# Performance work log

Measured on AMD Instinct MI355X. Metric: run time of the kernel, lower is better.

Reference implementation:

```python
import jax, jax.numpy as jnp
import numpy as np

N = 100000      # nodes
E = 1600000     # edges (avg degree 16)
IN_DIM = 128
HID = 128
OUT = 10
EPS = 1e-5      # BatchNorm eps


def _lin(key, fan_in, fan_out):
    return jax.random.normal(key, (fan_in, fan_out), jnp.float32) * (1.0 / np.sqrt(fan_in))


def setup_inputs() -> dict:
    key = jax.random.key(0)
    ks = jax.random.split(key, 8)
    x = jax.random.normal(ks[0], (N, IN_DIM), jnp.float32)
    edge_index = jax.random.randint(ks[1], (2, E), 0, N, dtype=jnp.int64)
    return {
        "x": x,
        "edge_index": edge_index,
        "W0": _lin(ks[2], IN_DIM, HID), "b0": jnp.zeros((HID,), jnp.float32),
        "g0": jnp.ones((HID,), jnp.float32), "be0": jnp.zeros((HID,), jnp.float32),
        "W1": _lin(ks[3], HID, HID), "b1": jnp.zeros((HID,), jnp.float32),
        "g1": jnp.ones((HID,), jnp.float32), "be1": jnp.zeros((HID,), jnp.float32),
        "W2": _lin(ks[4], HID, OUT), "b2": jnp.zeros((OUT,), jnp.float32),
    }


def gcn_conv(x, W, b, src, dst, n):
    # PyG GCNConv: add self-loops, symmetric normalization D^-1/2 A D^-1/2.
    # deg includes the self-loop (+1).
    e = src.shape[0]
    deg = jax.ops.segment_sum(jnp.ones((e,), x.dtype), dst, num_segments=n) + 1.0
    dinv = jax.lax.rsqrt(deg)                     # deg >= 1 always
    norm = dinv[src] * dinv[dst]                  # [E]
    h = x @ W                                     # [N, out]
    msgs = h[src] * norm[:, None]                 # gather + scale, [E, out]
    agg = jax.ops.segment_sum(msgs, dst, num_segments=n)
    agg = agg + h * (dinv * dinv)[:, None]        # self-loop contribution
    return agg + b


def batch_norm(x, gamma, beta):
    mu = jnp.mean(x, axis=0)
    var = jnp.mean(jnp.square(x - mu), axis=0)    # biased var, as torch BN training
    return gamma * (x - mu) * jax.lax.rsqrt(var + EPS) + beta


def reference(x, edge_index, W0, b0, g0, be0, W1, b1, g1, be1, W2, b2):
    src, dst = edge_index[0], edge_index[1]
    h = jax.nn.relu(batch_norm(gcn_conv(x, W0, b0, src, dst, N), g0, be0))
    h = jax.nn.relu(batch_norm(gcn_conv(h, W1, b1, src, dst, N), g1, be1))
    return gcn_conv(h, W2, b2, src, dst, N)
```

## Files before the change

kernel.cpp:

```cpp
#include <hip/hip_runtime.h>
#include <hip/hip_bf16.h>

static constexpr int NN  = 100000;
static constexpr int NE  = 1600000;
static constexpr int DIM = 128;
static constexpr int OC  = 10;
static constexpr int BK  = 64;
static constexpr float BN_EPS = 1e-5f;
static constexpr float INVN   = 1.0f / (float)NN;

typedef unsigned short ushortT;
typedef unsigned int uintT;
typedef __attribute__((ext_vector_type(8))) short short8;
typedef __attribute__((ext_vector_type(4))) float floatx4;

__device__ __forceinline__ ushortT f2bf(float f) {
    union { float f; unsigned int i; } c;
    c.f = f;
    unsigned int r = c.i + 0x7FFFu + ((c.i >> 16) & 1u);
    return (ushortT)(r >> 16);
}

__device__ __forceinline__ uintT pack2(float lo, float hi) {
    return (uintT)f2bf(lo) | ((uintT)f2bf(hi) << 16);
}

__device__ __forceinline__ float4 f4fma(const float4 w, const float s, const float4 acc) {
    float4 r;
    r.x = fmaf(w.x, s, acc.x);
    r.y = fmaf(w.y, s, acc.y);
    r.z = fmaf(w.z, s, acc.z);
    r.w = fmaf(w.w, s, acc.w);
    return r;
}

__device__ __forceinline__ void acc8(const uint4 u, float* a) {
    a[0] += __uint_as_float(u.x << 16);
    a[1] += __uint_as_float(u.x & 0xFFFF0000u);
    a[2] += __uint_as_float(u.y << 16);
    a[3] += __uint_as_float(u.y & 0xFFFF0000u);
    a[4] += __uint_as_float(u.z << 16);
    a[5] += __uint_as_float(u.z & 0xFFFF0000u);
    a[6] += __uint_as_float(u.w << 16);
    a[7] += __uint_as_float(u.w & 0xFFFF0000u);
}

__device__ __forceinline__ void fma8(const uint4 u, float s, float* a) {
    a[0] = fmaf(__uint_as_float(u.x << 16),          s, a[0]);
    a[1] = fmaf(__uint_as_float(u.x & 0xFFFF0000u),  s, a[1]);
    a[2] = fmaf(__uint_as_float(u.y << 16),          s, a[2]);
    a[3] = fmaf(__uint_as_float(u.y & 0xFFFF0000u),  s, a[3]);
    a[4] = fmaf(__uint_as_float(u.z << 16),          s, a[4]);
    a[5] = fmaf(__uint_as_float(u.z & 0xFFFF0000u),  s, a[5]);
    a[6] = fmaf(__uint_as_float(u.w << 16),          s, a[6]);
    a[7] = fmaf(__uint_as_float(u.w & 0xFFFF0000u),  s, a[7]);
}

__device__ __forceinline__ void unp8(const uint4 u, float* a) {
    a[0] = __uint_as_float(u.x << 16);
    a[1] = __uint_as_float(u.x & 0xFFFF0000u);
    a[2] = __uint_as_float(u.y << 16);
    a[3] = __uint_as_float(u.y & 0xFFFF0000u);
    a[4] = __uint_as_float(u.z << 16);
    a[5] = __uint_as_float(u.z & 0xFFFF0000u);
    a[6] = __uint_as_float(u.w << 16);
    a[7] = __uint_as_float(u.w & 0xFFFF0000u);
}

__global__ void k_wt(const float* __restrict__ W0, const float* __restrict__ W1,
                     ushortT* __restrict__ WT0, ushortT* __restrict__ WT1,
                     float* __restrict__ stats) {
    int i = blockIdx.x * 256 + threadIdx.x;
    if (i < 512) stats[i] = 0.f;
    int half = i >> 14, r = i & 16383;
    int n = r >> 7, k = r & 127;
    if (half == 0) WT0[r] = f2bf(W0[k * 128 + n]);
    else           WT1[r] = f2bf(W1[k * 128 + n]);
}

__global__ __launch_bounds__(256, 8)
void k_fused(const int* __restrict__ src, const int* __restrict__ dst,
             int* __restrict__ cnt, int* __restrict__ bucket,
             const float* __restrict__ x, const ushortT* __restrict__ WT,
             ushortT* __restrict__ outb)
{
    const int idx = blockIdx.x;
    const int m = idx / 3, r3 = idx - 3 * m;
    if (r3 < 2) {
        int e = (2 * m + r3) * 256 + threadIdx.x;
        if (e < NE) {
            int t = dst[e];
            int slot = atomicAdd(&cnt[t], 1);
            if (slot < BK)
                __hip_atomic_store(&bucket[(size_t)t * BK + slot], src[e],
                                   __ATOMIC_RELAXED, __HIP_MEMORY_SCOPE_AGENT);
        }
        return;
    }
    __shared__ ushortT XS[32 * 136];
    const int tid  = threadIdx.x;
    const int row0 = m * 32;

    #pragma unroll
    for (int i = 0; i < 4; ++i) {
        int id2 = tid + 256 * i;
        int rr = id2 >> 5, c4 = id2 & 31;
        int grow = row0 + rr;
        float4 v = {0.f, 0.f, 0.f, 0.f};
        if (grow < NN) v = ((const float4*)(x + (size_t)grow * DIM))[c4];
        ushort4 o;
        o.x = f2bf(v.x); o.y = f2bf(v.y); o.z = f2bf(v.z); o.w = f2bf(v.w);
        *(ushort4*)(XS + rr * 136 + c4 * 4) = o;
    }
    __syncthreads();

    const int w    = tid >> 6;
    const int lane = tid & 63;
    const int q    = lane >> 4;
    const int mr   = lane & 15;
    const int rw   = (w >> 1) * 16;
    const int ch   = (w & 1) * 64;

    floatx4 acc[4];
    #pragma unroll
    for (int t = 0; t < 4; ++t) { acc[t][0] = 0.f; acc[t][1] = 0.f; acc[t][2] = 0.f; acc[t][3] = 0.f; }

    #pragma unroll
    for (int c = 0; c < 4; ++c) {
        short8 a = *(const short8*)(XS + (rw + mr) * 136 + c * 32 + q * 8);
        #pragma unroll
        for (int t = 0; t < 4; ++t) {
            short8 b = *(const short8*)(WT + (size_t)(ch + t * 16 + mr) * 128 + c * 32 + q * 8);
            acc[t] = __builtin_amdgcn_mfma_f32_16x16x32_bf16(a, b, acc[t], 0, 0, 0);
        }
    }

    #pragma unroll
    for (int rr = 0; rr < 4; ++rr) {
        int grow = row0 + rw + q * 4 + rr;
        if (grow < NN) {
            #pragma unroll
            for (int t = 0; t < 4; ++t)
                outb[(size_t)grow * DIM + ch + t * 16 + mr] = f2bf(acc[t][rr]);
        }
    }
}

__global__ void k_dinv(const int* __restrict__ cnt, float* __restrict__ dinv, int n) {
    int i = blockIdx.x * 256 + threadIdx.x;
    if (i < n) dinv[i] = rsqrtf((float)cnt[i] + 1.0f);
}

template <bool EDGE_SCALE>
__global__ __launch_bounds__(256)
void k_agg_wide(const ushortT* __restrict__ hb, const int* __restrict__ cnt,
                const int* __restrict__ bucket, const float* __restrict__ dinv,
                const float* __restrict__ bias, ushortT* __restrict__ outBb,
                float* __restrict__ stats)
{
    const int lane = threadIdx.x & 63;
    const int w    = threadIdx.x >> 6;
    const int sg   = lane >> 4;
    const int f    = lane & 15;
    const int wid  = blockIdx.x * 4 + w;
    const int nW   = gridDim.x * 4;
    const uint4* h4 = (const uint4*)hb;

    float bl[8];
    #pragma unroll
    for (int i = 0; i < 8; ++i) bl[i] = bias[f * 8 + i];

    float ssum[8], ssq[8];
    #pragma unroll
    for (int i = 0; i < 8; ++i) { ssum[i] = 0.f; ssq[i] = 0.f; }

    for (int n = wid; n < NN; n += nW) {
        int d = cnt[n];
        if (d > BK) d = BK;
        const int* bp = bucket + (size_t)n * BK;
        float a[8];
        #pragma unroll
        for (int i = 0; i < 8; ++i) a[i] = 0.f;

        int j = 0;
        for (; j + 8 <= d; j += 8) {
            int s0 = bp[j + sg];
            int s1 = bp[j + 4 + sg];
            uint4 u0 = h4[(size_t)s0 * 16 + f];
            uint4 u1 = h4[(size_t)s1 * 16 + f];
            if (EDGE_SCALE) {
                float d0 = dinv[s0], d1 = dinv[s1];
                fma8(u0, d0, a);
                fma8(u1, d1, a);
            } else {
                acc8(u0, a);
                acc8(u1, a);
            }
        }
        for (; j < d; j += 4) {
            int e = j + sg;
            if (e < d) {
                int s0 = bp[e];
                uint4 u = h4[(size_t)s0 * 16 + f];
                if (EDGE_SCALE) fma8(u, dinv[s0], a);
                else            acc8(u, a);
            }
        }
        #pragma unroll
        for (int i = 0; i < 8; ++i) {
            a[i] += __shfl_xor(a[i], 16);
            a[i] += __shfl_xor(a[i], 32);
        }
        if (lane < 16) {
            uint4 us = h4[(size_t)n * 16 + f];
            float di = dinv[n];
            if (EDGE_SCALE) fma8(us, di, a);
            else            acc8(us, a);
            float v[8];
            #pragma unroll
            for (int i = 0; i < 8; ++i) v[i] = fmaf(di, a[i], bl[i]);
            uint4 o;
            o.x = pack2(v[0], v[1]);
            o.y = pack2(v[2], v[3]);
            o.z = pack2(v[4], v[5]);
            o.w = pack2(v[6], v[7]);
            ((uint4*)(outBb + (size_t)n * DIM))[f] = o;
            #pragma unroll
            for (int i = 0; i < 8; ++i) {
                ssum[i] += v[i];
                ssq[i]  = fmaf(v[i], v[i], ssq[i]);
            }
        }
    }

    __shared__ float ls[4 * 128], lq[4 * 128];
    if (lane < 16) {
        #pragma unroll
        for (int i = 0; i < 8; ++i) {
            ls[w * 128 + f * 8 + i] = ssum[i];
            lq[w * 128 + f * 8 + i] = ssq[i];
        }
    }
    __syncthreads();
    int t = threadIdx.x;
    if (t < 128) {
        float a = ls[t] + ls[128 + t] + ls[256 + t] + ls[384 + t];
        float b = lq[t] + lq[128 + t] + lq[256 + t] + lq[384 + t];
        unsafeAtomicAdd(&stats[t], a);
        unsafeAtomicAdd(&stats[128 + t], b);
    }
}

__global__ __launch_bounds__(256)
void k_mm128_l1(const ushortT* __restrict__ inb, const ushortT* __restrict__ WT,
                const float* __restrict__ stats, const float* __restrict__ g,
                const float* __restrict__ be, const float* __restrict__ dinv,
                ushortT* __restrict__ outb)
{
    __shared__ ushortT XS[64 * 136];
    __shared__ float CA[128], CD[128];
    const int tid  = threadIdx.x;
    const int row0 = blockIdx.x * 64;

    if (tid < 128) {
        float mu  = stats[tid] * INVN;
        float var = stats[128 + tid] * INVN - mu * mu;
        float a = g[tid] * rsqrtf(var + BN_EPS);
        CA[tid] = a;
        CD[tid] = be[tid] - mu * a;
    }
    __syncthreads();

    #pragma unroll
    for (int i = 0; i < 4; ++i) {
        int idx = tid + 256 * i;
        int r = idx >> 4, c8 = idx & 15;
        int grow = row0 + r;
        uint4 u = {0, 0, 0, 0};
        if (grow < NN) u = ((const uint4*)(inb + (size_t)grow * DIM))[c8];
        float v[8];
        unp8(u, v);
        #pragma unroll
        for (int k = 0; k < 8; ++k)
            v[k] = fmaxf(0.f, fmaf(v[k], CA[c8 * 8 + k], CD[c8 * 8 + k]));
        uint4 o;
        o.x = pack2(v[0], v[1]);
        o.y = pack2(v[2], v[3]);
        o.z = pack2(v[4], v[5]);
        o.w = pack2(v[6], v[7]);
        *(uint4*)(XS + r * 136 + c8 * 8) = o;
    }
    __syncthreads();

    const int w    = tid >> 6;
    const int lane = tid & 63;
    const int q    = lane >> 4;
    const int mr   = lane & 15;
    const int rw   = w * 16;

    floatx4 acc[8];
    #pragma unroll
    for (int t = 0; t < 8; ++t) { acc[t][0] = 0.f; acc[t][1] = 0.f; acc[t][2] = 0.f; acc[t][3] = 0.f; }

    #pragma unroll
    for (int c = 0; c < 4; ++c) {
        short8 a = *(const short8*)(XS + (rw + mr) * 136 + c * 32 + q * 8);
        #pragma unroll
        for (int t = 0; t < 8; ++t) {
            short8 b = *(const short8*)(WT + (size_t)(t * 16 + mr) * 128 + c * 32 + q * 8);
            acc[t] = __builtin_amdgcn_mfma_f32_16x16x32_bf16(a, b, acc[t], 0, 0, 0);
        }
    }

    #pragma unroll
    for (int r = 0; r < 4; ++r) {
        int grow = row0 + rw + q * 4 + r;
        if (grow < NN) {
            float di = dinv[grow];
            #pragma unroll
            for (int t = 0; t < 8; ++t) {
                outb[(size_t)grow * DIM + t * 16 + mr] = f2bf(acc[t][r] * di);
            }
        }
    }
}

__global__ __launch_bounds__(128)
void k_mm_l2(const ushortT* __restrict__ inb, const float* __restrict__ W2,
             const float* __restrict__ stats, const float* __restrict__ g,
             const float* __restrict__ be, const float* __restrict__ dinv,
             ushortT* __restrict__ Cb)
{
    __shared__ float WL[128 * 16];
    __shared__ float XS[32 * 128];
    __shared__ float CA[128], CD[128];
    const int tid  = threadIdx.x;
    const int row0 = blockIdx.x * 32;

    {
        float mu  = stats[tid] * INVN;
        float var = stats[128 + tid] * INVN - mu * mu;
        float a = g[tid] * rsqrtf(var + BN_EPS);
        CA[tid] = a;
        CD[tid] = be[tid] - mu * a;
    }
    for (int idx = tid; idx < 128 * 16; idx += 128) {
        int k = idx >> 4, c = idx & 15;
        WL[idx] = (c < OC) ? W2[k * OC + c] : 0.0f;
    }
    __syncthreads();

    #pragma unroll
    for (int i = 0; i < 4; ++i) {
        int idx = tid + 128 * i;
        int r = idx >> 4, c8 = idx & 15;
        uint4 u = ((const uint4*)(inb + (size_t)(row0 + r) * DIM))[c8];
        float v[8];
        unp8(u, v);
        float* xp = XS + r * 128 + c8 * 8;
        #pragma unroll
        for (int k = 0; k < 8; ++k)
            xp[k] = fmaxf(0.f, fmaf(v[k], CA[c8 * 8 + k], CD[c8 * 8 + k]));
    }
    __syncthreads();

    const int cg = tid & 3;
    const int rg = tid >> 2;
    float4 acc = {0, 0, 0, 0};
    const float4* XS4 = (const float4*)XS;
    const float4* WL4 = (const float4*)WL;
    for (int k = 0; k < 128; k += 4) {
        float4 w0 = WL4[(k + 0) * 4 + cg];
        float4 w1 = WL4[(k + 1) * 4 + cg];
        float4 w2 = WL4[(k + 2) * 4 + cg];
        float4 w3 = WL4[(k + 3) * 4 + cg];
        float4 x = XS4[rg * 32 + (k >> 2)];
        acc = f4fma(w0, x.x, f4fma(w1, x.y, f4fma(w2, x.z, f4fma(w3, x.w, acc))));
    }
    float di = dinv[row0 + rg];
    uint2 o;
    o.x = pack2(acc.x * di, acc.y * di);
    o.y = pack2(acc.z * di, acc.w * di);
    ((uint2*)(Cb + ((size_t)row0 + rg) * 16))[cg] = o;
}

__global__ __launch_bounds__(256)
void k_agg10(const ushortT* __restrict__ Cb, const int* __restrict__ cnt,
             const int* __restrict__ bucket, const float* __restrict__ dinv,
             const float* __restrict__ b2, float* __restrict__ out)
{
    const int lane = threadIdx.x & 63;
    const int sg   = lane >> 3;
    const int f    = lane & 7;
    const int wid  = (blockIdx.x * 256 + threadIdx.x) >> 6;
    const int nW   = gridDim.x * 4;
    const uintT* Cu = (const uintT*)Cb;

    for (int n = wid; n < NN; n += nW) {
        int d = cnt[n];
        if (d > BK) d = BK;
        const int* bp = bucket + (size_t)n * BK;
        float a0 = 0.f, a1 = 0.f;
        for (int j = sg; j < d; j += 8) {
            uintT u = Cu[(size_t)bp[j] * 8 + f];
            a0 += __uint_as_float(u << 16);
            a1 += __uint_as_float(u & 0xFFFF0000u);
        }
        a0 += __shfl_xor(a0, 8);  a1 += __shfl_xor(a1, 8);
        a0 += __shfl_xor(a0, 16); a1 += __shfl_xor(a1, 16);
        a0 += __shfl_xor(a0, 32); a1 += __shfl_xor(a1, 32);
        if (lane < 8) {
            uintT us = Cu[(size_t)n * 8 + f];
            a0 += __uint_as_float(us << 16);
            a1 += __uint_as_float(us & 0xFFFF0000u);
            float di = dinv[n];
            if (2 * f < OC) {
                float2 o;
                o.x = fmaf(di, a0, b2[2 * f]);
                o.y = fmaf(di, a1, b2[2 * f + 1]);
                *(float2*)(out + (size_t)n * OC + 2 * f) = o;
            }
        }
    }
}

extern "C" void kernel_launch(void* const* d_in, const int* in_sizes, int n_in,
                              void* d_out, int out_size, void* d_ws, size_t ws_size,
                              hipStream_t stream) {
    const float* x    = (const float*)d_in[0];
    const int*   ei   = (const int*)d_in[1];
    const int*   srcv = ei;
    const int*   dstv = ei + NE;
    const float* W0  = (const float*)d_in[2];
    const float* b0  = (const float*)d_in[3];
    const float* g0  = (const float*)d_in[4];
    const float* be0 = (const float*)d_in[5];
    const float* W1  = (const float*)d_in[6];
    const float* b1  = (const float*)d_in[7];
    const float* g1  = (const float*)d_in[8];
    const float* be1 = (const float*)d_in[9];
    const float* W2  = (const float*)d_in[10];
    const float* b2  = (const float*)d_in[11];
    float* out = (float*)d_out;

    float* base   = (float*)d_ws;
    int*   cnt    = (int*)base;
    float* dinv   = base + NN;
    float* stats  = base + 2 * NN;
    ushortT* WT0  = (ushortT*)(base + 2 * NN + 512);
    ushortT* WT1  = (ushortT*)(base + 2 * NN + 8704);
    int*   bucket = (int*)(base + 2 * NN + 16896);
    ushortT* A_bf = (ushortT*)(base + 2 * NN + 16896 + (size_t)NN * BK);
    ushortT* B_bf = A_bf + (size_t)NN * DIM;
    ushortT* Cb   = A_bf;

    hipMemsetAsync(cnt, 0, NN * sizeof(int), stream);

    k_wt<<<128, 256, 0, stream>>>(W0, W1, WT0, WT1, stats);

    k_fused<<<9375, 256, 0, stream>>>(srcv, dstv, cnt, bucket, x, WT0, A_bf);
    k_dinv<<<(NN + 255) / 256, 256, 0, stream>>>(cnt, dinv, NN);

    k_agg_wide<true><<<2048, 256, 0, stream>>>(A_bf, cnt, bucket, dinv, b0, B_bf, stats);

    k_mm128_l1<<<(NN + 63) / 64, 256, 0, stream>>>(B_bf, WT1, stats, g0, be0, dinv, A_bf);
    k_agg_wide<false><<<2048, 256, 0, stream>>>(A_bf, cnt, bucket, dinv, b1, B_bf, stats + 256);

    k_mm_l2<<<NN / 32, 128, 0, stream>>>(B_bf, W2, stats + 256, g1, be1, dinv, Cb);
    k_agg10<<<1024, 256, 0, stream>>>(Cb, cnt, bucket, dinv, b2, out);
}
```

Before: 560.5 us.

## Store hidden features in feature-sliced layout and aggregate per slice for cache locality

The GEMM outputs now write features in 8 slices of 16 columns each ([slice][node][16]), and the aggregation kernel assigns each block one slice and a contiguous node range, with 4 lanes per node. Each slice's working set (about 3.2 MB) is intended to fit in L2, so the random neighbour gathers hit cache more often than gathers over full 256-byte rows. In exchange, gathers shrink to 8 bytes per lane, the bucket indices are re-read once per slice, and the node-per-16-lane scheduling can diverge on degree imbalance.

```diff
diff --git a/kernel.cpp b/kernel.cpp
--- a/kernel.cpp
+++ b/kernel.cpp
@@ -9,6 +9,9 @@
 static constexpr float BN_EPS = 1e-5f;
 static constexpr float INVN   = 1.0f / (float)NN;
 
+static constexpr int NPB = (NN + 255) / 256;
+static constexpr int NPW = (NPB + 3) / 4;
+
 typedef unsigned short ushortT;
 typedef unsigned int uintT;
 typedef __attribute__((ext_vector_type(8))) short short8;
@@ -34,26 +37,11 @@
     return r;
 }
 
-__device__ __forceinline__ void acc8(const uint4 u, float* a) {
-    a[0] += __uint_as_float(u.x << 16);
-    a[1] += __uint_as_float(u.x & 0xFFFF0000u);
-    a[2] += __uint_as_float(u.y << 16);
-    a[3] += __uint_as_float(u.y & 0xFFFF0000u);
-    a[4] += __uint_as_float(u.z << 16);
-    a[5] += __uint_as_float(u.z & 0xFFFF0000u);
-    a[6] += __uint_as_float(u.w << 16);
-    a[7] += __uint_as_float(u.w & 0xFFFF0000u);
-}
-
-__device__ __forceinline__ void fma8(const uint4 u, float s, float* a) {
+__device__ __forceinline__ void fma4(const uint2 u, float s, float* a) {
     a[0] = fmaf(__uint_as_float(u.x << 16),          s, a[0]);
     a[1] = fmaf(__uint_as_float(u.x & 0xFFFF0000u),  s, a[1]);
     a[2] = fmaf(__uint_as_float(u.y << 16),          s, a[2]);
     a[3] = fmaf(__uint_as_float(u.y & 0xFFFF0000u),  s, a[3]);
-    a[4] = fmaf(__uint_as_float(u.z << 16),          s, a[4]);
-    a[5] = fmaf(__uint_as_float(u.z & 0xFFFF0000u),  s, a[5]);
-    a[6] = fmaf(__uint_as_float(u.w << 16),          s, a[6]);
-    a[7] = fmaf(__uint_as_float(u.w & 0xFFFF0000u),  s, a[7]);
 }
 
 __device__ __forceinline__ void unp8(const uint4 u, float* a) {
@@ -140,8 +128,9 @@
         int grow = row0 + rw + q * 4 + rr;
         if (grow < NN) {
             #pragma unroll
-            for (int t = 0; t < 4; ++t)
-                outb[(size_t)grow * DIM + ch + t * 16 + mr] = f2bf(acc[t][rr]);
+            for (int t = 0; t < 4; ++t) {
+                outb[(size_t)((ch >> 4) + t) * (NN * 16) + (size_t)grow * 16 + mr] = f2bf(acc[t][rr]);
+            }
         }
     }
 }
@@ -151,103 +140,89 @@
     if (i < n) dinv[i] = rsqrtf((float)cnt[i] + 1.0f);
 }
 
-template <bool EDGE_SCALE>
+template <bool ES>
 __global__ __launch_bounds__(256)
-void k_agg_wide(const ushortT* __restrict__ hb, const int* __restrict__ cnt,
-                const int* __restrict__ bucket, const float* __restrict__ dinv,
-                const float* __restrict__ bias, ushortT* __restrict__ outBb,
-                float* __restrict__ stats)
+void k_agg_slice(const ushortT* __restrict__ hb, const int* __restrict__ cnt,
+                 const int* __restrict__ bucket, const float* __restrict__ dinv,
+                 const float* __restrict__ bias, ushortT* __restrict__ outB,
+                 float* __restrict__ stats)
 {
+    const int s    = blockIdx.x & 7;
+    const int b    = blockIdx.x >> 3;
     const int lane = threadIdx.x & 63;
     const int w    = threadIdx.x >> 6;
-    const int sg   = lane >> 4;
-    const int f    = lane & 15;
-    const int wid  = blockIdx.x * 4 + w;
-    const int nW   = gridDim.x * 4;
-    const uint4* h4 = (const uint4*)hb;
-
-    float bl[8];
-    #pragma unroll
-    for (int i = 0; i < 8; ++i) bl[i] = bias[f * 8 + i];
-
-    float ssum[8], ssq[8];
-    #pragma unroll
-    for (int i = 0; i < 8; ++i) { ssum[i] = 0.f; ssq[i] = 0.f; }
-
-    for (int n = wid; n < NN; n += nW) {
-        int d = cnt[n];
-        if (d > BK) d = BK;
-        const int* bp = bucket + (size_t)n * BK;
-        float a[8];
-        #pragma unroll
-        for (int i = 0; i < 8; ++i) a[i] = 0.f;
-
-        int j = 0;
-        for (; j + 8 <= d; j += 8) {
-            int s0 = bp[j + sg];
-            int s1 = bp[j + 4 + sg];
-            uint4 u0 = h4[(size_t)s0 * 16 + f];
-            uint4 u1 = h4[(size_t)s1 * 16 + f];
-            if (EDGE_SCALE) {
-                float d0 = dinv[s0], d1 = dinv[s1];
-                fma8(u0, d0, a);
-                fma8(u1, d1, a);
-            } else {
-                acc8(u0, a);
-                acc8(u1, a);
+    const int ql   = lane >> 2;
+    const int fl   = lane & 3;
+    const ushortT* hsl = hb + (size_t)s * (NN * 16);
+
+    const int bStart = b * NPB;
+    const int bEnd   = (bStart + NPB < NN) ? bStart + NPB : NN;
+    const int wStart = bStart + w * NPW;
+    const int wEnd   = (wStart + NPW < bEnd) ? wStart + NPW : bEnd;
+
+    float bl[4];
+    #pragma unroll
+    for (int i = 0; i < 4; ++i) bl[i] = bias[s * 16 + fl * 4 + i];
+
+    float ssum[4] = {0.f, 0.f, 0.f, 0.f}, ssq[4] = {0.f, 0.f, 0.f, 0.f};
+
+    for (int nb = wStart; nb < wEnd; nb += 16) {
+        const int  n  = nb + ql;
+        const bool nv = (n < wEnd);
+        int d = 0;
+        if (nv) { d = cnt[n]; if (d > BK) d = BK; }
+        const int* bp = bucket + (size_t)(nv ? n : 0) * BK;
+
+        float a[4] = {0.f, 0.f, 0.f, 0.f};
+        for (int j = 0; ; j += 2) {
+            if (!__any(j < d)) break;
+            if (j < d) {
+                int2 pv = *(const int2*)(bp + j);
+                bool e1 = (j + 1 < d);
+                int s0 = pv.x;
+                int s1 = e1 ? pv.y : n;
+                uint2 u0 = *(const uint2*)(hsl + ((size_t)s0 << 4) + (fl << 2));
+                uint2 u1 = *(const uint2*)(hsl + ((size_t)s1 << 4) + (fl << 2));
+                float w0, w1;
+                if (ES) { w0 = dinv[s0]; w1 = e1 ? dinv[s1] : 0.f; }
+                else    { w0 = 1.f;      w1 = e1 ? 1.f      : 0.f; }
+                fma4(u0, w0, a);
+                fma4(u1, w1, a);
             }
         }
-        for (; j < d; j += 4) {
-            int e = j + sg;
-            if (e < d) {
-                int s0 = bp[e];
-                uint4 u = h4[(size_t)s0 * 16 + f];
-                if (EDGE_SCALE) fma8(u, dinv[s0], a);
-                else            acc8(u, a);
-            }
-        }
-        #pragma unroll
-        for (int i = 0; i < 8; ++i) {
-            a[i] += __shfl_xor(a[i], 16);
-            a[i] += __shfl_xor(a[i], 32);
-        }
-        if (lane < 16) {
-            uint4 us = h4[(size_t)n * 16 + f];
+        if (nv) {
+            uint2 us = *(const uint2*)(hsl + ((size_t)n << 4) + (fl << 2));
             float di = dinv[n];
-            if (EDGE_SCALE) fma8(us, di, a);
-            else            acc8(us, a);
-            float v[8];
+            fma4(us, ES ? di : 1.f, a);
+            float v[4];
             #pragma unroll
-            for (int i = 0; i < 8; ++i) v[i] = fmaf(di, a[i], bl[i]);
-            uint4 o;
+            for (int i = 0; i < 4; ++i) v[i] = fmaf(di, a[i], bl[i]);
+            uint2 o;
             o.x = pack2(v[0], v[1]);
             o.y = pack2(v[2], v[3]);
-            o.z = pack2(v[4], v[5]);
-            o.w = pack2(v[6], v[7]);
-            ((uint4*)(outBb + (size_t)n * DIM))[f] = o;
+            *(uint2*)(outB + (size_t)n * DIM + s * 16 + (fl << 2)) = o;
             #pragma unroll
-            for (int i = 0; i < 8; ++i) {
+            for (int i = 0; i < 4; ++i) {
                 ssum[i] += v[i];
                 ssq[i]  = fmaf(v[i], v[i], ssq[i]);
             }
         }
     }
 
-    __shared__ float ls[4 * 128], lq[4 * 128];
-    if (lane < 16) {
-        #pragma unroll
-        for (int i = 0; i < 8; ++i) {
-            ls[w * 128 + f * 8 + i] = ssum[i];
-            lq[w * 128 + f * 8 + i] = ssq[i];
-        }
-    }
-    __syncthreads();
-    int t = threadIdx.x;
-    if (t < 128) {
-        float a = ls[t] + ls[128 + t] + ls[256 + t] + ls[384 + t];
-        float b = lq[t] + lq[128 + t] + lq[256 + t] + lq[384 + t];
-        unsafeAtomicAdd(&stats[t], a);
-        unsafeAtomicAdd(&stats[128 + t], b);
+    #pragma unroll
+    for (int m = 4; m <= 32; m <<= 1) {
+        #pragma unroll
+        for (int i = 0; i < 4; ++i) {
+            ssum[i] += __shfl_xor(ssum[i], m);
+            ssq[i]  += __shfl_xor(ssq[i], m);
+        }
+    }
+    if (lane < 4) {
+        #pragma unroll
+        for (int i = 0; i < 4; ++i) {
+            unsafeAtomicAdd(&stats[s * 16 + fl * 4 + i], ssum[i]);
+            unsafeAtomicAdd(&stats[128 + s * 16 + fl * 4 + i], ssq[i]);
+        }
     }
 }
 
@@ -319,7 +294,7 @@
             float di = dinv[grow];
             #pragma unroll
             for (int t = 0; t < 8; ++t) {
-                outb[(size_t)grow * DIM + t * 16 + mr] = f2bf(acc[t][r] * di);
+                outb[(size_t)t * (NN * 16) + (size_t)grow * 16 + mr] = f2bf(acc[t][r] * di);
             }
         }
     }
@@ -461,10 +436,10 @@
     k_fused<<<9375, 256, 0, stream>>>(srcv, dstv, cnt, bucket, x, WT0, A_bf);
     k_dinv<<<(NN + 255) / 256, 256, 0, stream>>>(cnt, dinv, NN);
 
-    k_agg_wide<true><<<2048, 256, 0, stream>>>(A_bf, cnt, bucket, dinv, b0, B_bf, stats);
+    k_agg_slice<true><<<2048, 256, 0, stream>>>(A_bf, cnt, bucket, dinv, b0, B_bf, stats);
 
     k_mm128_l1<<<(NN + 63) / 64, 256, 0, stream>>>(B_bf, WT1, stats, g0, be0, dinv, A_bf);
-    k_agg_wide<false><<<2048, 256, 0, stream>>>(A_bf, cnt, bucket, dinv, b1, B_bf, stats + 256);
+    k_agg_slice<false><<<2048, 256, 0, stream>>>(A_bf, cnt, bucket, dinv, b1, B_bf, stats + 256);
 
     k_mm_l2<<<NN / 32, 128, 0, stream>>>(B_bf, W2, stats + 256, g1, be1, dinv, Cb);
     k_agg10<<<1024, 256, 0, stream>>>(Cb, cnt, bucket, dinv, b2, out);
```

Measured after the change: 771.5 us. 37.7% more time.

## Pad neighbor buckets to a sentinel row and aggregate two nodes per wave

Applied to the files above, without the earlier changes.

Edge bucketing now processes four edges per thread using vectorised int4 loads of src/dst. Each bucket is padded to a multiple of 16 with a sentinel index pointing at an added zero row, which has zero dinv. This lets aggregation read indices as int4 with no tail branches. Each wave now handles two nodes at once with eight independent gathers in flight, raising memory-level parallelism, at the cost of extra padded gathers and more registers.

```diff
diff --git a/kernel.cpp b/kernel.cpp
--- a/kernel.cpp
+++ b/kernel.cpp
@@ -69,9 +69,10 @@
 
 __global__ void k_wt(const float* __restrict__ W0, const float* __restrict__ W1,
                      ushortT* __restrict__ WT0, ushortT* __restrict__ WT1,
-                     float* __restrict__ stats) {
+                     float* __restrict__ stats, ushortT* __restrict__ hz) {
     int i = blockIdx.x * 256 + threadIdx.x;
     if (i < 512) stats[i] = 0.f;
+    if (i < DIM) hz[(size_t)NN * DIM + i] = 0;
     int half = i >> 14, r = i & 16383;
     int n = r >> 7, k = r & 127;
     if (half == 0) WT0[r] = f2bf(W0[k * 128 + n]);
@@ -85,18 +86,32 @@
              ushortT* __restrict__ outb)
 {
     const int idx = blockIdx.x;
-    const int m = idx / 3, r3 = idx - 3 * m;
-    if (r3 < 2) {
-        int e = (2 * m + r3) * 256 + threadIdx.x;
-        if (e < NE) {
-            int t = dst[e];
-            int slot = atomicAdd(&cnt[t], 1);
-            if (slot < BK)
-                __hip_atomic_store(&bucket[(size_t)t * BK + slot], src[e],
+    const int qq = idx / 3;
+    if (idx - 3 * qq == 0) {
+        int e0 = qq * 1024 + threadIdx.x * 4;
+        if (e0 < NE) {
+            int4 dv = *(const int4*)(dst + e0);
+            int4 sv = *(const int4*)(src + e0);
+            int t0 = atomicAdd(&cnt[dv.x], 1);
+            int t1 = atomicAdd(&cnt[dv.y], 1);
+            int t2 = atomicAdd(&cnt[dv.z], 1);
+            int t3 = atomicAdd(&cnt[dv.w], 1);
+            if (t0 < BK)
+                __hip_atomic_store(&bucket[(size_t)dv.x * BK + t0], sv.x,
                                    __ATOMIC_RELAXED, __HIP_MEMORY_SCOPE_AGENT);
+            if (t1 < BK)
+                __hip_atomic_store(&bucket[(size_t)dv.y * BK + t1], sv.y,
+                                   __ATOMIC_RELAXED, __HIP_MEMORY_SCOPE_AGENT);
+            if (t2 < BK)
+                __hip_atomic_store(&bucket[(size_t)dv.z * BK + t2], sv.z,
+                                   __ATOMIC_RELAXED, __HIP_MEMORY_SCOPE_AGENT);
+            if (t3 < BK)
+                __hip_atomic_store(&bucket[(size_t)dv.w * BK + t3], sv.w,
+                                   __ATOMIC_RELAXED, __HIP_MEMORY_SCOPE_AGENT);
         }
         return;
     }
+    const int m = idx - qq - 1;
     __shared__ ushortT XS[32 * 136];
     const int tid  = threadIdx.x;
     const int row0 = m * 32;
@@ -146,9 +161,19 @@
     }
 }
 
-__global__ void k_dinv(const int* __restrict__ cnt, float* __restrict__ dinv, int n) {
+__global__ void k_dinv(const int* __restrict__ cnt, float* __restrict__ dinv,
+                       int* __restrict__ bucket) {
     int i = blockIdx.x * 256 + threadIdx.x;
-    if (i < n) dinv[i] = rsqrtf((float)cnt[i] + 1.0f);
+    if (i < NN) {
+        int d = cnt[i];
+        dinv[i] = rsqrtf((float)d + 1.0f);
+        int dc = d > BK ? BK : d;
+        int dp = (dc + 15) & ~15;
+        int* bp = bucket + (size_t)i * BK;
+        for (int j = dc; j < dp; ++j) bp[j] = NN;
+    } else if (i == NN) {
+        dinv[NN] = 0.f;
+    }
 }
 
 template <bool EDGE_SCALE>
@@ -174,61 +199,109 @@
     #pragma unroll
     for (int i = 0; i < 8; ++i) { ssum[i] = 0.f; ssq[i] = 0.f; }
 
-    for (int n = wid; n < NN; n += nW) {
-        int d = cnt[n];
-        if (d > BK) d = BK;
-        const int* bp = bucket + (size_t)n * BK;
-        float a[8];
-        #pragma unroll
-        for (int i = 0; i < 8; ++i) a[i] = 0.f;
-
+    for (int n0 = wid * 2; n0 < NN; n0 += nW * 2) {
+        const int n1 = n0 + 1;
+        int2 dd = *(const int2*)(cnt + n0);
+        int d0 = dd.x > BK ? BK : dd.x;
+        int d1 = dd.y > BK ? BK : dd.y;
+        const int dp0 = (d0 + 15) & ~15;
+        const int dp1 = (d1 + 15) & ~15;
+        const int* bp0 = bucket + (size_t)n0 * BK;
+        const int* bp1 = bucket + (size_t)n1 * BK;
+
+        float a0[8], a1[8];
+        #pragma unroll
+        for (int i = 0; i < 8; ++i) { a0[i] = 0.f; a1[i] = 0.f; }
+
+        const int jc = dp0 < dp1 ? dp0 : dp1;
         int j = 0;
-        for (; j + 8 <= d; j += 8) {
-            int s0 = bp[j + sg];
-            int s1 = bp[j + 4 + sg];
-            uint4 u0 = h4[(size_t)s0 * 16 + f];
-            uint4 u1 = h4[(size_t)s1 * 16 + f];
+        for (; j < jc; j += 16) {
+            int4 p0 = *(const int4*)(bp0 + j + 4 * sg);
+            int4 p1 = *(const int4*)(bp1 + j + 4 * sg);
+            uint4 u00 = h4[(size_t)p0.x * 16 + f];
+            uint4 u01 = h4[(size_t)p0.y * 16 + f];
+            uint4 u02 = h4[(size_t)p0.z * 16 + f];
+            uint4 u03 = h4[(size_t)p0.w * 16 + f];
+            uint4 u10 = h4[(size_t)p1.x * 16 + f];
+            uint4 u11 = h4[(size_t)p1.y * 16 + f];
+            uint4 u12 = h4[(size_t)p1.z * 16 + f];
+            uint4 u13 = h4[(size_t)p1.w * 16 + f];
             if (EDGE_SCALE) {
-                float d0 = dinv[s0], d1 = dinv[s1];
-                fma8(u0, d0, a);
-                fma8(u1, d1, a);
+                fma8(u00, dinv[p0.x], a0);
+                fma8(u01, dinv[p0.y], a0);
+                fma8(u02, dinv[p0.z], a0);
+                fma8(u03, dinv[p0.w], a0);
+                fma8(u10, dinv[p1.x], a1);
+                fma8(u11, dinv[p1.y], a1);
+                fma8(u12, dinv[p1.z], a1);
+                fma8(u13, dinv[p1.w], a1);
             } else {
-                acc8(u0, a);
-                acc8(u1, a);
-            }
-        }
-        for (; j < d; j += 4) {
-            int e = j + sg;
-            if (e < d) {
-                int s0 = bp[e];
-                uint4 u = h4[(size_t)s0 * 16 + f];
-                if (EDGE_SCALE) fma8(u, dinv[s0], a);
-                else            acc8(u, a);
-            }
-        }
+                acc8(u00, a0); acc8(u01, a0); acc8(u02, a0); acc8(u03, a0);
+                acc8(u10, a1); acc8(u11, a1); acc8(u12, a1); acc8(u13, a1);
+            }
+        }
+        for (int j0 = j; j0 < dp0; j0 += 16) {
+            int4 p0 = *(const int4*)(bp0 + j0 + 4 * sg);
+            uint4 u00 = h4[(size_t)p0.x * 16 + f];
+            uint4 u01 = h4[(size_t)p0.y * 16 + f];
+            uint4 u02 = h4[(size_t)p0.z * 16 + f];
+            uint4 u03 = h4[(size_t)p0.w * 16 + f];
+            if (EDGE_SCALE) {
+                fma8(u00, dinv[p0.x], a0);
+                fma8(u01, dinv[p0.y], a0);
+                fma8(u02, dinv[p0.z], a0);
+                fma8(u03, dinv[p0.w], a0);
+            } else {
+                acc8(u00, a0); acc8(u01, a0); acc8(u02, a0); acc8(u03, a0);
+            }
+        }
+        for (int j1 = j; j1 < dp1; j1 += 16) {
+            int4 p1 = *(const int4*)(bp1 + j1 + 4 * sg);
+            uint4 u10 = h4[(size_t)p1.x * 16 + f];
+            uint4 u11 = h4[(size_t)p1.y * 16 + f];
+            uint4 u12 = h4[(size_t)p1.z * 16 + f];
+            uint4 u13 = h4[(size_t)p1.w * 16 + f];
+            if (EDGE_SCALE) {
+                fma8(u10, dinv[p1.x], a1);
+                fma8(u11, dinv[p1.y], a1);
+                fma8(u12, dinv[p1.z], a1);
+                fma8(u13, dinv[p1.w], a1);
+            } else {
+                acc8(u10, a1); acc8(u11, a1); acc8(u12, a1); acc8(u13, a1);
+            }
+        }
+
         #pragma unroll
         for (int i = 0; i < 8; ++i) {
-            a[i] += __shfl_xor(a[i], 16);
-            a[i] += __shfl_xor(a[i], 32);
+            a0[i] += __shfl_xor(a0[i], 16);
+            a0[i] += __shfl_xor(a0[i], 32);
+            a1[i] += __shfl_xor(a1[i], 16);
+            a1[i] += __shfl_xor(a1[i], 32);
         }
         if (lane < 16) {
-            uint4 us = h4[(size_t)n * 16 + f];
-            float di = dinv[n];
-            if (EDGE_SCALE) fma8(us, di, a);
-            else            acc8(us, a);
-            float v[8];
-            #pragma unroll
-            for (int i = 0; i < 8; ++i) v[i] = fmaf(di, a[i], bl[i]);
-            uint4 o;
-            o.x = pack2(v[0], v[1]);
-            o.y = pack2(v[2], v[3]);
-            o.z = pack2(v[4], v[5]);
-            o.w = pack2(v[6], v[7]);
-            ((uint4*)(outBb + (size_t)n * DIM))[f] = o;
+            uint4 us0 = h4[(size_t)n0 * 16 + f];
+            uint4 us1 = h4[(size_t)n1 * 16 + f];
+            float2 dv2 = *(const float2*)(dinv + n0);
+            if (EDGE_SCALE) { fma8(us0, dv2.x, a0); fma8(us1, dv2.y, a1); }
+            else            { acc8(us0, a0);        acc8(us1, a1); }
+            float v0[8], v1[8];
             #pragma unroll
             for (int i = 0; i < 8; ++i) {
-                ssum[i] += v[i];
-                ssq[i]  = fmaf(v[i], v[i], ssq[i]);
+                v0[i] = fmaf(dv2.x, a0[i], bl[i]);
+                v1[i] = fmaf(dv2.y, a1[i], bl[i]);
+            }
+            uint4 o0, o1;
+            o0.x = pack2(v0[0], v0[1]); o0.y = pack2(v0[2], v0[3]);
+            o0.z = pack2(v0[4], v0[5]); o0.w = pack2(v0[6], v0[7]);
+            o1.x = pack2(v1[0], v1[1]); o1.y = pack2(v1[2], v1[3]);
+            o1.z = pack2(v1[4], v1[5]); o1.w = pack2(v1[6], v1[7]);
+            ((uint4*)(outBb + (size_t)n0 * DIM))[f] = o0;
+            ((uint4*)(outBb + (size_t)n1 * DIM))[f] = o1;
+            #pragma unroll
+            for (int i = 0; i < 8; ++i) {
+                ssum[i] += v0[i] + v1[i];
+                ssq[i]   = fmaf(v0[i], v0[i], ssq[i]);
+                ssq[i]   = fmaf(v1[i], v1[i], ssq[i]);
             }
         }
     }
@@ -446,20 +519,20 @@
     float* base   = (float*)d_ws;
     int*   cnt    = (int*)base;
     float* dinv   = base + NN;
-    float* stats  = base + 2 * NN;
-    ushortT* WT0  = (ushortT*)(base + 2 * NN + 512);
-    ushortT* WT1  = (ushortT*)(base + 2 * NN + 8704);
-    int*   bucket = (int*)(base + 2 * NN + 16896);
-    ushortT* A_bf = (ushortT*)(base + 2 * NN + 16896 + (size_t)NN * BK);
-    ushortT* B_bf = A_bf + (size_t)NN * DIM;
+    float* stats  = base + 2 * NN + 4;
+    ushortT* WT0  = (ushortT*)(base + 2 * NN + 516);
+    ushortT* WT1  = (ushortT*)(base + 2 * NN + 8708);
+    int*   bucket = (int*)(base + 2 * NN + 16900);
+    ushortT* A_bf = (ushortT*)(base + 2 * NN + 16900 + (size_t)NN * BK);
+    ushortT* B_bf = A_bf + (size_t)(NN + 1) * DIM;
     ushortT* Cb   = A_bf;
 
-    hipMemsetAsync(cnt, 0, NN * sizeof(int), stream);
-
-    k_wt<<<128, 256, 0, stream>>>(W0, W1, WT0, WT1, stats);
-
-    k_fused<<<9375, 256, 0, stream>>>(srcv, dstv, cnt, bucket, x, WT0, A_bf);
-    k_dinv<<<(NN + 255) / 256, 256, 0, stream>>>(cnt, dinv, NN);
+    (void)hipMemsetAsync(cnt, 0, NN * sizeof(int), stream);
+
+    k_wt<<<128, 256, 0, stream>>>(W0, W1, WT0, WT1, stats, A_bf);
+
+    k_fused<<<4688, 256, 0, stream>>>(srcv, dstv, cnt, bucket, x, WT0, A_bf);
+    k_dinv<<<(NN + 256) / 256, 256, 0, stream>>>(cnt, dinv, bucket);
 
     k_agg_wide<true><<<2048, 256, 0, stream>>>(A_bf, cnt, bucket, dinv, b0, B_bf, stats);
 
```

Result: slower. 648.3 us (+15.7%).
